# Performance work log

Hardware: AMD Instinct MI355X
Metric: run time of the kernel (lower is better)

## Reference

```python
import jax, jax.numpy as jnp
from jax import lax
import numpy as np

LRELU_SLOPE = 0.2
DEMOD_EPS = 1e-8


def _mod_conv(x, style, weight, bias, demodulate, pad):
    """StyleGAN2 modulated conv via grouped conv (groups = batch).
    x: [B,Cin,H,W]; style: [B,Cin]; weight: [Cout,Cin,kh,kw]; bias: [Cout]."""
    B, Cin, H, W = x.shape
    Cout, _, kh, kw = weight.shape
    # per-sample modulated weight [B,Cout,Cin,kh,kw]
    wt = weight[None] * style[:, None, :, None, None]
    if demodulate:
        wt = wt / jnp.sqrt(jnp.sum(wt ** 2, axis=(2, 3, 4), keepdims=True) + DEMOD_EPS)
    out = lax.conv_general_dilated(
        x.reshape(1, B * Cin, H, W),
        wt.reshape(B * Cout, Cin, kh, kw),
        window_strides=(1, 1),
        padding=[(pad, pad), (pad, pad)],
        dimension_numbers=('NCHW', 'OIHW', 'NCHW'),
        feature_group_count=B,
    )
    return out.reshape(B, Cout, H, W) + bias[None, :, None, None]


def setup_inputs() -> dict:
    key = jax.random.key(0)
    ks = jax.random.split(key, 16)
    B, Cin, Cout, Wd, H = 4, 512, 256, 512, 64
    f32 = jnp.float32
    d = {
        'x': jax.random.normal(ks[0], (B, Cin, H, H), f32),
        'w': jax.random.normal(ks[1], (B, Wd), f32),
        # conv1: Cin->Cout 3x3
        'w1': jax.random.normal(ks[2], (Cout, Cin, 3, 3), f32) / np.float32(np.sqrt(Cin * 9)),
        'b1': jax.random.normal(ks[3], (Cout,), f32) * 0.01,
        'a1w': jax.random.normal(ks[4], (Cin, Wd), f32) / np.float32(np.sqrt(Wd)),
        'a1b': jnp.ones((Cin,), f32),
        # conv2: Cout->Cout 3x3
        'w2': jax.random.normal(ks[5], (Cout, Cout, 3, 3), f32) / np.float32(np.sqrt(Cout * 9)),
        'b2': jax.random.normal(ks[6], (Cout,), f32) * 0.01,
        'a2w': jax.random.normal(ks[7], (Cout, Wd), f32) / np.float32(np.sqrt(Wd)),
        'a2b': jnp.ones((Cout,), f32),
        # to_rgb: Cout->3 1x1, no demodulation
        'w3': jax.random.normal(ks[8], (3, Cout, 1, 1), f32) / np.float32(np.sqrt(Cout)),
        'b3': jax.random.normal(ks[9], (3,), f32) * 0.01,
        'a3w': jax.random.normal(ks[10], (Cout, Wd), f32) / np.float32(np.sqrt(Wd)),
        'a3b': jnp.ones((Cout,), f32),
    }
    return d


def reference(x, w, w1, b1, a1w, a1b, w2, b2, a2w, a2b, w3, b3, a3w, a3b):
    B, C, H, W = x.shape
    # nn.Upsample(scale_factor=2, mode='bilinear', align_corners=False) == half-pixel bilinear
    xu = jax.image.resize(x, (B, C, 2 * H, 2 * W), method='bilinear')
    s1 = w @ a1w.T + a1b                      # affine -> per-sample style [B,Cin]
    h = jax.nn.leaky_relu(_mod_conv(xu, s1, w1, b1, True, 1), LRELU_SLOPE)
    s2 = w @ a2w.T + a2b
    h = jax.nn.leaky_relu(_mod_conv(h, s2, w2, b2, True, 1), LRELU_SLOPE)
    s3 = w @ a3w.T + a3b
    rgb = jax.nn.leaky_relu(_mod_conv(h, s3, w3, b3, False, 0), LRELU_SLOPE)
    return (h, rgb)
```

## Files before the change

kernel.cpp:

```cpp
#include <hip/hip_runtime.h>
#include <stdint.h>

typedef __attribute__((ext_vector_type(8))) short bhalf8;
typedef __attribute__((ext_vector_type(4))) float fx4;

__device__ __forceinline__ unsigned short f2bf(float f) {
    unsigned u = __builtin_bit_cast(unsigned, f);
    unsigned r = (u + 0x7fffu + ((u >> 16) & 1u)) >> 16;
    return (unsigned short)r;
}
__device__ __forceinline__ float bf2f(unsigned short h) {
    unsigned u = ((unsigned)h) << 16;
    return __builtin_bit_cast(float, u);
}
__device__ __forceinline__ float lrelu(float v) { return v > 0.f ? v : 0.2f * v; }

typedef __attribute__((address_space(1))) void as1_void;
typedef __attribute__((address_space(3))) void as3_void;
__device__ __forceinline__ void gl_lds16(const void* g, void* l) {
    __builtin_amdgcn_global_load_lds((as1_void*)(void*)g, (as3_void*)l, 16, 0, 0);
}

__global__ __launch_bounds__(256) void style_kernel(
    const float* __restrict__ w,
    const float* __restrict__ a1w, const float* __restrict__ a1b,
    const float* __restrict__ a2w, const float* __restrict__ a2b,
    const float* __restrict__ a3w, const float* __restrict__ a3b,
    float* __restrict__ s1, float* __restrict__ s2, float* __restrict__ s3)
{
    int gw = blockIdx.x * 4 + (threadIdx.x >> 6);
    int lane = threadIdx.x & 63;
    int b = gw >> 10, r = gw & 1023;
    const float* arow; const float* abias; float* dst;
    if (r < 512)      { arow = a1w + (size_t)r * 512;        abias = a1b + r;       dst = s1 + b * 512 + r; }
    else if (r < 768) { int rr = r - 512; arow = a2w + (size_t)rr * 512; abias = a2b + rr; dst = s2 + b * 256 + rr; }
    else              { int rr = r - 768; arow = a3w + (size_t)rr * 512; abias = a3b + rr; dst = s3 + b * 256 + rr; }
    const float* wrow = w + b * 512;
    float acc = 0.f;
    #pragma unroll
    for (int j = 0; j < 8; ++j) {
        int c = lane + j * 64;
        acc += wrow[c] * arow[c];
    }
    #pragma unroll
    for (int off = 32; off; off >>= 1) acc += __shfl_down(acc, off, 64);
    if (lane == 0) *dst = acc + *abias;
}

__global__ __launch_bounds__(256) void demod_kernel(
    const float* __restrict__ w1, const float* __restrict__ w2,
    const float* __restrict__ s1, const float* __restrict__ s2,
    float* __restrict__ d1, float* __restrict__ d2)
{
    int blk = blockIdx.x;
    int conv = blk >> 10, b = (blk >> 8) & 3, o = blk & 255;
    int t = threadIdx.x;
    int cin = conv ? 256 : 512;
    const float* s = conv ? (s2 + b * 256) : (s1 + b * 512);
    const float* row = (conv ? w2 : w1) + (size_t)o * cin * 9;
    __shared__ float sv[512];
    for (int i = t; i < cin; i += 256) { float v = s[i]; sv[i] = v * v; }
    __syncthreads();
    float sum = 0.f;
    int n = cin * 9;
    for (int k = t; k < n; k += 256) {
        float v = row[k];
        sum += v * v * sv[k / 9];
    }
    #pragma unroll
    for (int off = 32; off; off >>= 1) sum += __shfl_down(sum, off, 64);
    __shared__ float red[4];
    if ((t & 63) == 0) red[t >> 6] = sum;
    __syncthreads();
    if (t == 0) {
        float tot = red[0] + red[1] + red[2] + red[3];
        (conv ? d2 : d1)[b * 256 + o] = rsqrtf(tot + 1e-8f);
    }
}

__global__ __launch_bounds__(256) void pack_kernel(
    const float* __restrict__ w1, const float* __restrict__ w2,
    unsigned short* __restrict__ wp1, unsigned short* __restrict__ wp2)
{
    int tid = blockIdx.x * 256 + threadIdx.x;
    const int N1 = 1179648, N2 = 589824;
    if (tid < N1) {
        int e = tid & 7, m = (tid >> 3) & 127, kh = (tid >> 10) & 3;
        int dx = (tid >> 12) % 3, ic = (tid / 12288) & 15;
        int dy = (tid / 196608) % 3, mblk = tid / 589824;
        int o = mblk * 128 + m, ci = ic * 32 + kh * 8 + e;
        wp1[tid] = f2bf(w1[((size_t)o * 512 + ci) * 9 + dy * 3 + dx]);
    } else if (tid < N1 + N2) {
        int t2 = tid - N1;
        int e = t2 & 7, m = (t2 >> 3) & 127, kh = (t2 >> 10) & 3;
        int dx = (t2 >> 12) % 3, ic = (t2 / 12288) & 7;
        int dy = (t2 / 98304) % 3, mblk = t2 / 294912;
        int o = mblk * 128 + m, ci = ic * 32 + kh * 8 + e;
        wp2[t2] = f2bf(w2[((size_t)o * 256 + ci) * 9 + dy * 3 + dx]);
    }
}

__global__ __launch_bounds__(256) void upsample_kernel(
    const float* __restrict__ x, const float* __restrict__ s1,
    unsigned short* __restrict__ xu)
{
    __shared__ float L[2][64][65];
    int bid = blockIdx.x, t = threadIdx.x;
    int yo = bid & 127, b = bid >> 7;
    int k = yo >> 1;
    int sy0, sy1; float wy0, wy1;
    if ((yo & 1) == 0) { sy0 = k > 0 ? k - 1 : 0; sy1 = k; wy0 = 0.25f; wy1 = 0.75f; }
    else               { sy0 = k; sy1 = k < 63 ? k + 1 : 63; wy0 = 0.75f; wy1 = 0.25f; }
    for (int c0 = 0; c0 < 512; c0 += 64) {
        __syncthreads();
        #pragma unroll
        for (int j = 0; j < 32; ++j) {
            int f = t + j * 256;
            int idx = f & 63, rowid = f >> 6;
            int cc = rowid & 63, which = rowid >> 6;
            int sy = which ? sy1 : sy0;
            L[which][cc][idx] = x[((size_t)(b * 512 + c0 + cc) * 64 + sy) * 64 + idx];
        }
        __syncthreads();
        #pragma unroll
        for (int j = 0; j < 16; ++j) {
            int it = t + j * 256;
            int cp = it & 31, xo = it >> 5;
            int kk = xo >> 1, sx0, sx1; float wx0, wx1;
            if ((xo & 1) == 0) { sx0 = kk > 0 ? kk - 1 : 0; sx1 = kk; wx0 = 0.25f; wx1 = 0.75f; }
            else               { sx0 = kk; sx1 = kk < 63 ? kk + 1 : 63; wx0 = 0.75f; wx1 = 0.25f; }
            int c = cp * 2;
            float A0 = wx0 * L[0][c][sx0] + wx1 * L[0][c][sx1];
            float B0 = wx0 * L[1][c][sx0] + wx1 * L[1][c][sx1];
            float A1 = wx0 * L[0][c + 1][sx0] + wx1 * L[0][c + 1][sx1];
            float B1 = wx0 * L[1][c + 1][sx0] + wx1 * L[1][c + 1][sx1];
            float v0 = (wy0 * A0 + wy1 * B0) * s1[b * 512 + c0 + c];
            float v1 = (wy0 * A1 + wy1 * B1) * s1[b * 512 + c0 + c + 1];
            unsigned pk = (unsigned)f2bf(v0) | ((unsigned)f2bf(v1) << 16);
            *(unsigned*)&xu[((size_t)(b * 128 + yo) * 128 + xo) * 512 + c0 + c] = pk;
        }
    }
}

template<int CIN, bool IS_CONV2>
__global__ __launch_bounds__(512, 4) void conv3x3_kernel(
    const unsigned short* __restrict__ inp,
    const unsigned short* __restrict__ wpack,
    const float* __restrict__ dvec,
    const float* __restrict__ bias,
    const float* __restrict__ post,
    unsigned short* __restrict__ outmod,
    float* __restrict__ outf)
{
    constexpr int NIC = CIN / 32;
    __shared__ __attribute__((aligned(16))) short Alds[2][12288];
    __shared__ __attribute__((aligned(16))) short Blds[4][128][32];
    const int tid = threadIdx.x;
    const int lane = tid & 63;
    const int wvi = tid >> 6;
    const int bid = blockIdx.x;
    const int y0 = (bid & 63) << 1;
    const int mblk = (bid >> 6) & 1;
    const int b = bid >> 7;
    const int wm = (wvi >> 2) * 64;
    const int row = (wvi >> 1) & 1;
    const int wn = (wvi & 1) * 64;
    const int lhi = lane >> 4;
    const int llo = lane & 15;

    const int xg = tid >> 2, i8 = tid & 3;
    const int i8s = i8 ^ ((xg >> 1) & 3);

    fx4 acc[4][4];
    #pragma unroll
    for (int mt = 0; mt < 4; ++mt)
        #pragma unroll
        for (int nt = 0; nt < 4; ++nt) acc[mt][nt] = (fx4){0.f, 0.f, 0.f, 0.f};

    auto stageB = [&](int ic) {
        #pragma unroll
        for (int rr = 0; rr < 4; ++rr) {
            const int yy = y0 - 1 + rr;
            char* dstB = (char*)&Blds[rr][0][0] + tid * 16;
            if ((unsigned)yy < 128u) {
                gl_lds16(inp + ((size_t)(b * 128 + yy) * 128 + xg) * CIN + ic * 32 + i8s * 8, dstB);
            } else {
                *(int4*)dstB = make_int4(0, 0, 0, 0);
            }
        }
    };
    auto stageA = [&](int ic, int dy, int buf) {
        const unsigned short* asrc = wpack + ((size_t)(mblk * 3 + dy) * NIC + ic) * 12288;
        #pragma unroll
        for (int j = 0; j < 3; ++j) {
            int g = tid + j * 512;
            gl_lds16(asrc + (size_t)g * 8, (char*)&Alds[buf][0] + g * 16);
        }
    };

    stageB(0);
    stageA(0, 0, 0);
    __syncthreads();

    int par = 0;
    for (int ic = 0; ic < NIC; ++ic) {
        #pragma unroll
        for (int dy = 0; dy < 3; ++dy) {
            const bool last = (ic == NIC - 1) && (dy == 2);
            if (!last) {
                const int nic = (dy == 2) ? ic + 1 : ic;
                const int ndy = (dy == 2) ? 0 : dy + 1;
                stageA(nic, ndy, par ^ 1);
            }
            const short* Ab = &Alds[par][0];
            const short* Brow = &Blds[row + dy][0][0];
            #pragma unroll
            for (int dx = 0; dx < 3; ++dx) {
                bhalf8 af[4], bfr[4];
                #pragma unroll
                for (int mt = 0; mt < 4; ++mt)
                    af[mt] = *(const bhalf8*)&Ab[dx * 4096 + (lhi * 128 + wm + mt * 16 + llo) * 8];
                #pragma unroll
                for (int nt = 0; nt < 4; ++nt) {
                    const int s = wn + nt * 16 + llo + dx;
                    if ((nt == 0 && dx == 0) || (nt == 3 && dx == 2)) {
                        const bool edge = (s == 0) || (s == 129);
                        const int sp = edge ? 0 : (s - 1);
                        const int key = (sp >> 1) & 3;
                        bhalf8 v = *(const bhalf8*)&Brow[sp * 32 + ((lhi ^ key) << 3)];
                        bhalf8 z = {0, 0, 0, 0, 0, 0, 0, 0};
                        bfr[nt] = edge ? z : v;
                    } else {
                        const int sp = s - 1;
                        const int key = (sp >> 1) & 3;
                        bfr[nt] = *(const bhalf8*)&Brow[sp * 32 + ((lhi ^ key) << 3)];
                    }
                }
                __builtin_amdgcn_s_setprio(1);
                #pragma unroll
                for (int mt = 0; mt < 4; ++mt)
                    #pragma unroll
                    for (int nt = 0; nt < 4; ++nt)
                        acc[mt][nt] = __builtin_amdgcn_mfma_f32_16x16x32_bf16(
                            af[mt], bfr[nt], acc[mt][nt], 0, 0, 0);
                __builtin_amdgcn_s_setprio(0);
            }
            if (dy == 2 && ic + 1 < NIC) {
                __syncthreads();
                stageB(ic + 1);
            }
            if (!last) __syncthreads();
            par ^= 1;
        }
    }

    const int y = y0 + row;
    #pragma unroll
    for (int mt = 0; mt < 4; ++mt) {
        const int o0 = mblk * 128 + wm + mt * 16 + lhi * 4;
        const fx4 d4 = *(const fx4*)(dvec + b * 256 + o0);
        const fx4 bb4 = *(const fx4*)(bias + o0);
        const fx4 p4 = *(const fx4*)(post + b * 256 + o0);
        #pragma unroll
        for (int nt = 0; nt < 4; ++nt) {
            const int xo = wn + nt * 16 + llo;
            unsigned lo = 0, hi = 0;
            #pragma unroll
            for (int r = 0; r < 4; ++r) {
                float v = acc[mt][nt][r] * d4[r] + bb4[r];
                v = lrelu(v);
                if (IS_CONV2)
                    outf[(((size_t)b * 256 + o0 + r) * 128 + y) * 128 + xo] = v;
                unsigned short ub = f2bf(v * p4[r]);
                if (r < 2) lo |= (unsigned)ub << (16 * r);
                else       hi |= (unsigned)ub << (16 * (r - 2));
            }
            *(uint2*)&outmod[((size_t)(b * 128 + y) * 128 + xo) * 256 + o0] = make_uint2(lo, hi);
        }
    }
}

__global__ __launch_bounds__(256) void rgb_kernel(
    const unsigned short* __restrict__ hs3,
    const float* __restrict__ w3, const float* __restrict__ b3,
    float* __restrict__ out)
{
    __shared__ float wl[768];
    int t = threadIdx.x;
    for (int i = t; i < 768; i += 256) wl[i] = w3[i];
    __syncthreads();
    int p = blockIdx.x * 64 + (t >> 2);
    int q = t & 3;
    const unsigned short* src = hs3 + (size_t)p * 256 + q * 64;
    float a0 = 0.f, a1 = 0.f, a2 = 0.f;
    #pragma unroll
    for (int c8 = 0; c8 < 64; c8 += 8) {
        int4 pk = *(const int4*)(src + c8);
        #pragma unroll
        for (int qq = 0; qq < 4; ++qq) {
            unsigned uu = ((const unsigned*)&pk)[qq];
            float ve = bf2f((unsigned short)(uu & 0xffffu));
            float vo = bf2f((unsigned short)(uu >> 16));
            int c = q * 64 + c8 + qq * 2;
            a0 += ve * wl[c] + vo * wl[c + 1];
            a1 += ve * wl[256 + c] + vo * wl[256 + c + 1];
            a2 += ve * wl[512 + c] + vo * wl[512 + c + 1];
        }
    }
    a0 += __shfl_xor(a0, 1, 64); a0 += __shfl_xor(a0, 2, 64);
    a1 += __shfl_xor(a1, 1, 64); a1 += __shfl_xor(a1, 2, 64);
    a2 += __shfl_xor(a2, 1, 64); a2 += __shfl_xor(a2, 2, 64);
    int b = p >> 14, yx = p & 16383;
    if (q < 3) {
        float v = (q == 0) ? a0 : (q == 1) ? a1 : a2;
        out[((size_t)b * 3 + q) * 16384 + yx] = lrelu(v + b3[q]);
    }
}

extern "C" void kernel_launch(void* const* d_in, const int* in_sizes, int n_in,
                              void* d_out, int out_size, void* d_ws, size_t ws_size,
                              hipStream_t stream) {
    const float* x   = (const float*)d_in[0];
    const float* w   = (const float*)d_in[1];
    const float* w1  = (const float*)d_in[2];
    const float* b1  = (const float*)d_in[3];
    const float* a1w = (const float*)d_in[4];
    const float* a1b = (const float*)d_in[5];
    const float* w2  = (const float*)d_in[6];
    const float* b2  = (const float*)d_in[7];
    const float* a2w = (const float*)d_in[8];
    const float* a2b = (const float*)d_in[9];
    const float* w3  = (const float*)d_in[10];
    const float* b3  = (const float*)d_in[11];
    const float* a3w = (const float*)d_in[12];
    const float* a3b = (const float*)d_in[13];

    char* ws = (char*)d_ws;
    unsigned short* xu  = (unsigned short*)(ws);
    unsigned short* hs3 = (unsigned short*)(ws);
    unsigned short* t1  = (unsigned short*)(ws + 67108864);
    unsigned short* wp1 = (unsigned short*)(ws + 100663296);
    unsigned short* wp2 = (unsigned short*)(ws + 103022592);
    float* s1 = (float*)(ws + 104202240);
    float* s2 = (float*)(ws + 104210432);
    float* s3 = (float*)(ws + 104214528);
    float* d1 = (float*)(ws + 104218624);
    float* d2 = (float*)(ws + 104222720);

    float* h_out   = (float*)d_out;
    float* rgb_out = h_out + 16777216;

    style_kernel<<<1024, 256, 0, stream>>>(w, a1w, a1b, a2w, a2b, a3w, a3b, s1, s2, s3);
    demod_kernel<<<2048, 256, 0, stream>>>(w1, w2, s1, s2, d1, d2);
    pack_kernel<<<6912, 256, 0, stream>>>(w1, w2, wp1, wp2);
    upsample_kernel<<<512, 256, 0, stream>>>(x, s1, xu);
    conv3x3_kernel<512, false><<<512, 512, 0, stream>>>(xu, wp1, d1, b1, s2, t1, nullptr);
    conv3x3_kernel<256, true><<<512, 512, 0, stream>>>(t1, wp2, d2, b2, s3, hs3, h_out);
    rgb_kernel<<<1024, 256, 0, stream>>>(hs3, w3, b3, rgb_out);
}
```

Before: 370.4 us.

## Restructure upsample kernel with transposed LDS tile and vectorized loads and stores

```diff
diff --git a/kernel.cpp b/kernel.cpp
--- a/kernel.cpp
+++ b/kernel.cpp
@@ -104,40 +104,71 @@
     const float* __restrict__ x, const float* __restrict__ s1,
     unsigned short* __restrict__ xu)
 {
-    __shared__ float L[2][64][65];
-    int bid = blockIdx.x, t = threadIdx.x;
-    int yo = bid & 127, b = bid >> 7;
-    int k = yo >> 1;
-    int sy0, sy1; float wy0, wy1;
-    if ((yo & 1) == 0) { sy0 = k > 0 ? k - 1 : 0; sy1 = k; wy0 = 0.25f; wy1 = 0.75f; }
-    else               { sy0 = k; sy1 = k < 63 ? k + 1 : 63; wy0 = 0.75f; wy1 = 0.25f; }
-    for (int c0 = 0; c0 < 512; c0 += 64) {
-        __syncthreads();
-        #pragma unroll
-        for (int j = 0; j < 32; ++j) {
-            int f = t + j * 256;
-            int idx = f & 63, rowid = f >> 6;
-            int cc = rowid & 63, which = rowid >> 6;
-            int sy = which ? sy1 : sy0;
-            L[which][cc][idx] = x[((size_t)(b * 512 + c0 + cc) * 64 + sy) * 64 + idx];
-        }
-        __syncthreads();
-        #pragma unroll
-        for (int j = 0; j < 16; ++j) {
-            int it = t + j * 256;
-            int cp = it & 31, xo = it >> 5;
-            int kk = xo >> 1, sx0, sx1; float wx0, wx1;
+    __shared__ float Lt[3][64][68];
+    const int bid = blockIdx.x;
+    const int cch = bid & 7, k = (bid >> 3) & 63, b = bid >> 9;
+    const int c0 = cch * 64;
+    const int t = threadIdx.x;
+
+    {
+        const int px4 = t & 15, cc4 = t >> 4;
+        #pragma unroll
+        for (int r = 0; r < 3; ++r) {
+            int sy = k - 1 + r; sy = sy < 0 ? 0 : (sy > 63 ? 63 : sy);
+            float4 v[4];
+            #pragma unroll
+            for (int j = 0; j < 4; ++j)
+                v[j] = *(const float4*)&x[((size_t)(b * 512 + c0 + cc4 * 4 + j) * 64 + sy) * 64 + px4 * 4];
+            #pragma unroll
+            for (int o = 0; o < 4; ++o) {
+                fx4 w4;
+                w4[0] = ((const float*)&v[0])[o];
+                w4[1] = ((const float*)&v[1])[o];
+                w4[2] = ((const float*)&v[2])[o];
+                w4[3] = ((const float*)&v[3])[o];
+                *(fx4*)&Lt[r][px4 * 4 + o][cc4 * 4] = w4;
+            }
+        }
+    }
+    __syncthreads();
+
+    const int oct = t & 7, xob = t >> 3;
+    float sty[8];
+    #pragma unroll
+    for (int j = 0; j < 8; ++j) sty[j] = s1[b * 512 + c0 + oct * 8 + j];
+
+    #pragma unroll
+    for (int half = 0; half < 2; ++half) {
+        const int yo = 2 * k + half;
+        const int rA = half ? 1 : 0, rB = rA + 1;
+        const float wyA = half ? 0.75f : 0.25f, wyB = half ? 0.25f : 0.75f;
+        #pragma unroll
+        for (int i = 0; i < 4; ++i) {
+            const int xo = xob + i * 32;
+            const int kk = xo >> 1;
+            int sx0, sx1; float wx0, wx1;
             if ((xo & 1) == 0) { sx0 = kk > 0 ? kk - 1 : 0; sx1 = kk; wx0 = 0.25f; wx1 = 0.75f; }
             else               { sx0 = kk; sx1 = kk < 63 ? kk + 1 : 63; wx0 = 0.75f; wx1 = 0.25f; }
-            int c = cp * 2;
-            float A0 = wx0 * L[0][c][sx0] + wx1 * L[0][c][sx1];
-            float B0 = wx0 * L[1][c][sx0] + wx1 * L[1][c][sx1];
-            float A1 = wx0 * L[0][c + 1][sx0] + wx1 * L[0][c + 1][sx1];
-            float B1 = wx0 * L[1][c + 1][sx0] + wx1 * L[1][c + 1][sx1];
-            float v0 = (wy0 * A0 + wy1 * B0) * s1[b * 512 + c0 + c];
-            float v1 = (wy0 * A1 + wy1 * B1) * s1[b * 512 + c0 + c + 1];
-            unsigned pk = (unsigned)f2bf(v0) | ((unsigned)f2bf(v1) << 16);
-            *(unsigned*)&xu[((size_t)(b * 128 + yo) * 128 + xo) * 512 + c0 + c] = pk;
+            unsigned pk[4];
+            #pragma unroll
+            for (int h = 0; h < 2; ++h) {
+                const fx4 a0 = *(const fx4*)&Lt[rA][sx0][oct * 8 + h * 4];
+                const fx4 a1 = *(const fx4*)&Lt[rA][sx1][oct * 8 + h * 4];
+                const fx4 b0 = *(const fx4*)&Lt[rB][sx0][oct * 8 + h * 4];
+                const fx4 b1 = *(const fx4*)&Lt[rB][sx1][oct * 8 + h * 4];
+                #pragma unroll
+                for (int j2 = 0; j2 < 2; ++j2) {
+                    float v0 = wyA * (wx0 * a0[j2 * 2]     + wx1 * a1[j2 * 2])
+                             + wyB * (wx0 * b0[j2 * 2]     + wx1 * b1[j2 * 2]);
+                    float v1 = wyA * (wx0 * a0[j2 * 2 + 1] + wx1 * a1[j2 * 2 + 1])
+                             + wyB * (wx0 * b0[j2 * 2 + 1] + wx1 * b1[j2 * 2 + 1]);
+                    v0 *= sty[h * 4 + j2 * 2];
+                    v1 *= sty[h * 4 + j2 * 2 + 1];
+                    pk[h * 2 + j2] = (unsigned)f2bf(v0) | ((unsigned)f2bf(v1) << 16);
+                }
+            }
+            *(int4*)&xu[((size_t)(b * 128 + yo) * 128 + xo) * 512 + c0 + oct * 8] =
+                make_int4(pk[0], pk[1], pk[2], pk[3]);
         }
     }
 }
@@ -353,7 +384,7 @@
     style_kernel<<<1024, 256, 0, stream>>>(w, a1w, a1b, a2w, a2b, a3w, a3b, s1, s2, s3);
     demod_kernel<<<2048, 256, 0, stream>>>(w1, w2, s1, s2, d1, d2);
     pack_kernel<<<6912, 256, 0, stream>>>(w1, w2, wp1, wp2);
-    upsample_kernel<<<512, 256, 0, stream>>>(x, s1, xu);
+    upsample_kernel<<<2048, 256, 0, stream>>>(x, s1, xu);
     conv3x3_kernel<512, false><<<512, 512, 0, stream>>>(xu, wp1, d1, b1, s2, t1, nullptr);
     conv3x3_kernel<256, true><<<512, 512, 0, stream>>>(t1, wp2, d2, b2, s3, hs3, h_out);
     rgb_kernel<<<1024, 256, 0, stream>>>(hs3, w3, b3, rgb_out);
```

New measurement: 361.9 us. 2.3% less time.
